# Kernel tuning notes

Measured on AMD Instinct MI355X. Metric: run time of the kernel, lower is better.

Reference implementation:

```python
import jax, jax.numpy as jnp
import numpy as np

NUM_GRAPHS = 256


def _lin_params(key, fan_in, fan_out):
    k1, k2 = jax.random.split(key)
    bound = 1.0 / np.sqrt(fan_in)
    W = jax.random.uniform(k1, (fan_in, fan_out), jnp.float32, -bound, bound)
    b = jax.random.uniform(k2, (fan_out,), jnp.float32, -bound, bound)
    return W, b


def setup_inputs() -> dict:
    key = jax.random.key(0)
    ks = jax.random.split(key, 12)
    N, E, F = 100000, 3200000, 32
    x = jax.random.normal(ks[0], (N, F), jnp.float32)
    edge_index = jax.random.randint(ks[1], (2, E), 0, N, jnp.int64)
    batch = jnp.sort(jax.random.randint(ks[2], (N,), 0, NUM_GRAPHS, jnp.int64))
    W1, b1 = _lin_params(ks[3], 32, 32)   # conv1
    W2, b2 = _lin_params(ks[4], 32, 24)   # conv2
    Wg, bg = _lin_params(ks[5], 24, 32)   # g_fcn1
    Wt, bt = _lin_params(ks[6], 32, 2)    # t_fcn1
    Wn1, bn1 = _lin_params(ks[7], 24, 16)  # n_fcn1
    Wn2, bn2 = _lin_params(ks[8], 16, 1)   # n_fcn2
    Wb1, bb1 = _lin_params(ks[9], 24, 16)  # b_fcn1
    Wb2, bb2 = _lin_params(ks[10], 16, 3)  # b_fcn2
    return {"x": x, "edge_index": edge_index, "batch": batch,
            "W1": W1, "b1": b1, "W2": W2, "b2": b2,
            "Wg": Wg, "bg": bg, "Wt": Wt, "bt": bt,
            "Wn1": Wn1, "bn1": bn1, "Wn2": Wn2, "bn2": bn2,
            "Wb1": Wb1, "bb1": bb1, "Wb2": Wb2, "bb2": bb2}


def _gcn_conv(x, edge_index, W, b):
    """PyG GCNConv: self-loops + symmetric normalization + linear."""
    N = x.shape[0]
    h = x @ W  # [N, out]
    loop = jnp.arange(N, dtype=edge_index.dtype)
    row = jnp.concatenate([edge_index[0], loop])  # source
    col = jnp.concatenate([edge_index[1], loop])  # target
    deg = jax.ops.segment_sum(jnp.ones_like(col, dtype=h.dtype), col, num_segments=N)
    dinv = jnp.where(deg > 0, jax.lax.rsqrt(deg), 0.0)
    norm = dinv[row] * dinv[col]  # [E+N]
    out = jax.ops.segment_sum(h[row] * norm[:, None], col, num_segments=N)
    return out + b


def _segment_softmax(v, seg, num_seg):
    """Softmax over nodes within each graph (leading axis)."""
    m = jax.ops.segment_max(v, seg, num_segments=num_seg)
    e = jnp.exp(v - m[seg])
    s = jax.ops.segment_sum(e, seg, num_segments=num_seg)
    return e / s[seg]


def reference(x, edge_index, batch, W1, b1, W2, b2, Wg, bg, Wt, bt,
              Wn1, bn1, Wn2, bn2, Wb1, bb1, Wb2, bb2):
    h = jax.nn.relu(_gcn_conv(x, edge_index, W1, b1))          # [N,32]
    h = jax.nn.relu(_gcn_conv(h, edge_index, W2, b2))          # [N,24]
    # global mean pool
    cnt = jax.ops.segment_sum(jnp.ones((h.shape[0],), h.dtype), batch, num_segments=NUM_GRAPHS)
    g = jax.ops.segment_sum(h, batch, num_segments=NUM_GRAPHS) / jnp.maximum(cnt, 1.0)[:, None]
    g = g @ Wg + bg                                            # [G,32]
    t = jax.nn.softmax(g @ Wt + bt, axis=1)                    # [G,2]
    n = jax.nn.relu(h @ Wn1 + bn1) @ Wn2 + bn2                 # [N,1]
    n = _segment_softmax(n, batch, NUM_GRAPHS)                 # per-graph softmax over nodes
    b_feat = jax.ops.segment_sum(n * h, batch, num_segments=NUM_GRAPHS)  # global_add_pool of n*x
    bb = jax.nn.relu(b_feat @ Wb1 + bb1) @ Wb2 + bb2           # [G,3]
    bb = jax.nn.softmax(bb, axis=0)                            # dim=0 softmax as in source
    return (t, n, bb)
```

## Files before the change

kernel.cpp:

```cpp
#include <hip/hip_runtime.h>
#include <math.h>

#define NG 256
#define NBLK 256

#define S1F 16.0f
#define IS1F 0.0625f
#define S2F 64.0f
#define IS2F 0.015625f

typedef __attribute__((ext_vector_type(2))) float f32x2;

__device__ __forceinline__ unsigned enc4(float f0, float f1, float f2, float f3) {
    int r = __builtin_amdgcn_cvt_pk_fp8_f32(f0, f1, 0, false);
    r = __builtin_amdgcn_cvt_pk_fp8_f32(f2, f3, r, true);
    return (unsigned)r;
}
__device__ __forceinline__ void acc8p(uint2 v, f32x2 (&a)[4]) {
    a[0] += __builtin_amdgcn_cvt_pk_f32_fp8((int)v.x, false);
    a[1] += __builtin_amdgcn_cvt_pk_f32_fp8((int)v.x, true);
    a[2] += __builtin_amdgcn_cvt_pk_f32_fp8((int)v.y, false);
    a[3] += __builtin_amdgcn_cvt_pk_f32_fp8((int)v.y, true);
}

__global__ __launch_bounds__(256) void hist_bucket_kernel(
        const int* __restrict__ col, int* __restrict__ blockOff,
        int* __restrict__ bucketTot, int E, int NB) {
    __shared__ int h[512];
    h[threadIdx.x] = 0; h[threadIdx.x + 256] = 0;
    __syncthreads();
    const int chunk = (((E + NBLK - 1) / NBLK) + 3) & ~3;
    const int beg = blockIdx.x * chunk;
    const int end = min(beg + chunk, E);
    if ((E & 3) == 0) {
        int e = beg + threadIdx.x * 4;
        for (; e + 3 < end; e += 1024) {
            int4 c = *(const int4*)(col + e);
            atomicAdd(&h[c.x >> 8], 1);
            atomicAdd(&h[c.y >> 8], 1);
            atomicAdd(&h[c.z >> 8], 1);
            atomicAdd(&h[c.w >> 8], 1);
        }
        for (; e < end; e++) atomicAdd(&h[col[e] >> 8], 1);
    } else {
        for (int e = beg + threadIdx.x; e < end; e += 256)
            atomicAdd(&h[col[e] >> 8], 1);
    }
    __syncthreads();
    for (int t = threadIdx.x; t < NB; t += 256) {
        int off = atomicAdd(&bucketTot[t], h[t]);
        blockOff[t * NBLK + blockIdx.x] = off;
    }
}

__global__ __launch_bounds__(512) void tiny_scan_kernel(
        const int* __restrict__ bucketTot, int* __restrict__ bucketBase, int NB) {
    __shared__ int part[512];
    const int t = threadIdx.x;
    int v = (t < NB) ? bucketTot[t] : 0;
    part[t] = v;
    __syncthreads();
    for (int o = 1; o < 512; o <<= 1) {
        int u = (t >= o) ? part[t - o] : 0;
        __syncthreads();
        part[t] += u;
        __syncthreads();
    }
    if (t < NB) bucketBase[t] = part[t] - v;
    if (t == NB) bucketBase[NB] = part[NB - 1];
    if (t == 511 && NB == 512) bucketBase[NB] = part[511];
}

__global__ __launch_bounds__(256) void scatter_pairs_kernel(
        const int* __restrict__ ei, const int* __restrict__ blockOff,
        const int* __restrict__ bucketBase, int* __restrict__ pairs, int E, int NB) {
    __shared__ int cur[512];
    for (int t = threadIdx.x; t < NB; t += 256)
        cur[t] = bucketBase[t] + blockOff[t * NBLK + blockIdx.x];
    __syncthreads();
    const int chunk = (((E + NBLK - 1) / NBLK) + 3) & ~3;
    const int beg = blockIdx.x * chunk;
    const int end = min(beg + chunk, E);
    if ((E & 3) == 0) {
        int e = beg + threadIdx.x * 4;
        for (; e + 3 < end; e += 1024) {
            int4 s = *(const int4*)(ei + e);
            int4 tg = *(const int4*)(ei + E + e);
            int p0 = atomicAdd(&cur[tg.x >> 8], 1);
            pairs[p0] = (int)(((unsigned)(tg.x & 255) << 17) | (unsigned)s.x);
            int p1 = atomicAdd(&cur[tg.y >> 8], 1);
            pairs[p1] = (int)(((unsigned)(tg.y & 255) << 17) | (unsigned)s.y);
            int p2 = atomicAdd(&cur[tg.z >> 8], 1);
            pairs[p2] = (int)(((unsigned)(tg.z & 255) << 17) | (unsigned)s.z);
            int p3 = atomicAdd(&cur[tg.w >> 8], 1);
            pairs[p3] = (int)(((unsigned)(tg.w & 255) << 17) | (unsigned)s.w);
        }
        for (; e < end; e++) {
            int src = ei[e];
            int tgt = ei[E + e];
            int pos = atomicAdd(&cur[tgt >> 8], 1);
            pairs[pos] = (int)(((unsigned)(tgt & 255) << 17) | (unsigned)src);
        }
    } else {
        for (int e = beg + threadIdx.x; e < end; e += 256) {
            int src = ei[e];
            int tgt = ei[E + e];
            int pos = atomicAdd(&cur[tgt >> 8], 1);
            pairs[pos] = (int)(((unsigned)(tgt & 255) << 17) | (unsigned)src);
        }
    }
}

__global__ __launch_bounds__(256) void csr_bucket_kernel(
        const int* __restrict__ pairs, const int* __restrict__ bucketBase,
        int* __restrict__ rowptr, int* __restrict__ adj,
        float* __restrict__ dinv, int N, int E) {
    __shared__ int h[256];
    __shared__ int sc[256];
    __shared__ int cur[256];
    const int b = blockIdx.x, t = threadIdx.x;
    const int base = bucketBase[b];
    const int end = bucketBase[b + 1];
    h[t] = 0;
    __syncthreads();
    for (int i = base + t; i < end; i += 256)
        atomicAdd(&h[(unsigned)pairs[i] >> 17], 1);
    __syncthreads();
    const int v = h[t];
    sc[t] = v;
    __syncthreads();
    for (int o = 1; o < 256; o <<= 1) {
        int u = (t >= o) ? sc[t - o] : 0;
        __syncthreads();
        sc[t] += u;
        __syncthreads();
    }
    const int ex = sc[t] - v;
    const int node = (b << 8) + t;
    if (node < N) {
        rowptr[node] = base + ex;
        dinv[node] = rsqrtf((float)v + 1.0f);
    }
    cur[t] = base + ex;
    __syncthreads();
    for (int i = base + t; i < end; i += 256) {
        unsigned p = (unsigned)pairs[i];
        int pos = atomicAdd(&cur[p >> 17], 1);
        adj[pos] = (int)(p & 0x1FFFFu);
    }
    if (b == 0 && t == 0) rowptr[N] = E;
}

__global__ __launch_bounds__(256) void bounds_kernel(
        const int* __restrict__ batch, int* __restrict__ starts, int N) {
    int i = blockIdx.x * blockDim.x + threadIdx.x;
    if (i >= N) return;
    int b = batch[i];
    int bp = (i == 0) ? -1 : batch[i - 1];
    for (int g = bp + 1; g <= b; g++) starts[g] = i;
    if (i == N - 1)
        for (int g = b + 1; g <= NG; g++) starts[g] = N;
}

__global__ __launch_bounds__(256) void hs1_kernel(
        const float* __restrict__ x, const float* __restrict__ W,
        const float* __restrict__ dinv, unsigned* __restrict__ hs, int N) {
    __shared__ float Ws[32 * 32];
    __shared__ float tmp[8][32];
    for (int t = threadIdx.x; t < 1024; t += blockDim.x) Ws[t] = W[t];
    __syncthreads();
    const int tid = threadIdx.x;
    const int node = blockIdx.x * 8 + (tid >> 5);
    const int n = tid >> 5, f = tid & 31;
    if (node < N) {
        const float* xr = x + (size_t)node * 32;
        float acc = 0.f;
#pragma unroll
        for (int k = 0; k < 32; k++) acc += xr[k] * Ws[k * 32 + f];
        tmp[n][f] = acc * dinv[node] * S1F;
        if (f < 8)
            hs[(size_t)node * 8 + f] = enc4(tmp[n][4 * f], tmp[n][4 * f + 1],
                                            tmp[n][4 * f + 2], tmp[n][4 * f + 3]);
    }
}

__global__ __launch_bounds__(256) void gather1_kernel(
        const int* __restrict__ rowptr, const int* __restrict__ adj,
        const uint2* __restrict__ hs1q, const float* __restrict__ dinv,
        const float* __restrict__ b1, const float* __restrict__ W2,
        unsigned* __restrict__ hs2out, int N) {
    __shared__ float W2s[32 * 24];
    __shared__ float b1s[32];
    __shared__ float h1row[8][32];
    __shared__ float hs2t[8][32];
    const int tid = threadIdx.x;
    for (int t = tid; t < 768; t += 256) W2s[t] = W2[t];
    if (tid < 32) b1s[tid] = b1[tid];

    const int node = blockIdx.x * 8 + (tid >> 5);
    const int n = tid >> 5;
    const int l = tid & 31;
    const int f8 = l & 3;
    const int e8 = l >> 2;
    const bool valid = node < N;

    int beg = 0, cnt = 0;
    if (valid) { beg = rowptr[node]; cnt = rowptr[node + 1] - beg; }
    const int* ap = adj + beg;
    f32x2 a[4];
#pragma unroll
    for (int k = 0; k < 4; k++) { a[k][0] = 0.f; a[k][1] = 0.f; }
    int j = 0;
    for (; j + 32 <= cnt; j += 32) {
        int s0 = ap[j + e8];
        int s1 = ap[j + 8 + e8];
        int s2 = ap[j + 16 + e8];
        int s3 = ap[j + 24 + e8];
        uint2 v0 = hs1q[(size_t)s0 * 4 + f8];
        uint2 v1 = hs1q[(size_t)s1 * 4 + f8];
        uint2 v2 = hs1q[(size_t)s2 * 4 + f8];
        uint2 v3 = hs1q[(size_t)s3 * 4 + f8];
        acc8p(v0, a); acc8p(v1, a); acc8p(v2, a); acc8p(v3, a);
    }
    for (; j + 16 <= cnt; j += 16) {
        int s0 = ap[j + e8];
        int s1 = ap[j + 8 + e8];
        uint2 v0 = hs1q[(size_t)s0 * 4 + f8];
        uint2 v1 = hs1q[(size_t)s1 * 4 + f8];
        acc8p(v0, a); acc8p(v1, a);
    }
    for (; j + 8 <= cnt; j += 8) {
        int s0 = ap[j + e8];
        acc8p(hs1q[(size_t)s0 * 4 + f8], a);
    }
    if (e8 < cnt - j) {
        int s0 = ap[j + e8];
        acc8p(hs1q[(size_t)s0 * 4 + f8], a);
    }
#pragma unroll
    for (int k = 0; k < 4; k++) {
        float x0 = a[k][0], x1 = a[k][1];
        x0 += __shfl_xor(x0, 4); x0 += __shfl_xor(x0, 8); x0 += __shfl_xor(x0, 16);
        x1 += __shfl_xor(x1, 4); x1 += __shfl_xor(x1, 8); x1 += __shfl_xor(x1, 16);
        a[k][0] = x0; a[k][1] = x1;
    }

    __syncthreads();

    float di = 0.f;
    if (valid) {
        di = dinv[node];
        if (e8 == 0) {
            f32x2 s[4];
#pragma unroll
            for (int k = 0; k < 4; k++) { s[k][0] = 0.f; s[k][1] = 0.f; }
            acc8p(hs1q[(size_t)node * 4 + f8], s);
            const float c = di * IS1F;
#pragma unroll
            for (int k = 0; k < 4; k++) {
                h1row[n][8 * f8 + 2 * k]     = fmaxf(c * (a[k][0] + s[k][0]) + b1s[8 * f8 + 2 * k], 0.f);
                h1row[n][8 * f8 + 2 * k + 1] = fmaxf(c * (a[k][1] + s[k][1]) + b1s[8 * f8 + 2 * k + 1], 0.f);
            }
        }
    }
    if (valid) {
        float aa = 0.f;
        if (l < 24) {
#pragma unroll
            for (int k = 0; k < 32; k++) aa += h1row[n][k] * W2s[k * 24 + l];
        }
        hs2t[n][l] = (l < 24) ? aa * di * S2F : 0.f;
        if (l < 8)
            hs2out[(size_t)node * 8 + l] = enc4(hs2t[n][4 * l], hs2t[n][4 * l + 1],
                                                hs2t[n][4 * l + 2], hs2t[n][4 * l + 3]);
    }
}

__global__ __launch_bounds__(256) void gather2_kernel(
        const int* __restrict__ rowptr, const int* __restrict__ adj,
        const uint2* __restrict__ hs2q, const float* __restrict__ dinv,
        const float* __restrict__ b2,
        const float* __restrict__ Wn1, const float* __restrict__ bn1,
        const float* __restrict__ Wn2, const float* __restrict__ bn2,
        float* __restrict__ h2out, float* __restrict__ vout, int N) {
    __shared__ float Wn1s[24 * 16];
    __shared__ float b2s[32], bn1s[16], Wn2s[16];
    __shared__ float h2row[8][32];
    const int tid = threadIdx.x;
    for (int t = tid; t < 384; t += 256) Wn1s[t] = Wn1[t];
    if (tid < 32) b2s[tid] = (tid < 24) ? b2[tid] : 0.f;
    if (tid < 16) { bn1s[tid] = bn1[tid]; Wn2s[tid] = Wn2[tid]; }

    const int node = blockIdx.x * 8 + (tid >> 5);
    const int n = tid >> 5;
    const int l = tid & 31;
    const int f8 = l & 3;
    const int e8 = l >> 2;
    const bool valid = node < N;

    int beg = 0, cnt = 0;
    if (valid) { beg = rowptr[node]; cnt = rowptr[node + 1] - beg; }
    const int* ap = adj + beg;
    f32x2 a[4];
#pragma unroll
    for (int k = 0; k < 4; k++) { a[k][0] = 0.f; a[k][1] = 0.f; }
    int j = 0;
    for (; j + 32 <= cnt; j += 32) {
        int s0 = ap[j + e8];
        int s1 = ap[j + 8 + e8];
        int s2 = ap[j + 16 + e8];
        int s3 = ap[j + 24 + e8];
        uint2 v0 = hs2q[(size_t)s0 * 4 + f8];
        uint2 v1 = hs2q[(size_t)s1 * 4 + f8];
        uint2 v2 = hs2q[(size_t)s2 * 4 + f8];
        uint2 v3 = hs2q[(size_t)s3 * 4 + f8];
        acc8p(v0, a); acc8p(v1, a); acc8p(v2, a); acc8p(v3, a);
    }
    for (; j + 16 <= cnt; j += 16) {
        int s0 = ap[j + e8];
        int s1 = ap[j + 8 + e8];
        uint2 v0 = hs2q[(size_t)s0 * 4 + f8];
        uint2 v1 = hs2q[(size_t)s1 * 4 + f8];
        acc8p(v0, a); acc8p(v1, a);
    }
    for (; j + 8 <= cnt; j += 8) {
        int s0 = ap[j + e8];
        acc8p(hs2q[(size_t)s0 * 4 + f8], a);
    }
    if (e8 < cnt - j) {
        int s0 = ap[j + e8];
        acc8p(hs2q[(size_t)s0 * 4 + f8], a);
    }
#pragma unroll
    for (int k = 0; k < 4; k++) {
        float x0 = a[k][0], x1 = a[k][1];
        x0 += __shfl_xor(x0, 4); x0 += __shfl_xor(x0, 8); x0 += __shfl_xor(x0, 16);
        x1 += __shfl_xor(x1, 4); x1 += __shfl_xor(x1, 8); x1 += __shfl_xor(x1, 16);
        a[k][0] = x0; a[k][1] = x1;
    }

    __syncthreads();

    if (valid && e8 == 0) {
        float di = dinv[node];
        f32x2 s[4];
#pragma unroll
        for (int k = 0; k < 4; k++) { s[k][0] = 0.f; s[k][1] = 0.f; }
        acc8p(hs2q[(size_t)node * 4 + f8], s);
        const float c = di * IS2F;
#pragma unroll
        for (int k = 0; k < 4; k++) {
            h2row[n][8 * f8 + 2 * k]     = fmaxf(c * (a[k][0] + s[k][0]) + b2s[8 * f8 + 2 * k], 0.f);
            h2row[n][8 * f8 + 2 * k + 1] = fmaxf(c * (a[k][1] + s[k][1]) + b2s[8 * f8 + 2 * k + 1], 0.f);
        }
    }
    if (valid && l < 24) h2out[(size_t)node * 24 + l] = h2row[n][l];

    float val = 0.f;
    if (valid && l < 16) {
        float u = bn1s[l];
#pragma unroll
        for (int k = 0; k < 24; k++) u += h2row[n][k] * Wn1s[k * 16 + l];
        val = fmaxf(u, 0.f) * Wn2s[l];
    }
    val += __shfl_down(val, 8, 16);
    val += __shfl_down(val, 4, 16);
    val += __shfl_down(val, 2, 16);
    val += __shfl_down(val, 1, 16);
    if (valid && l == 0) vout[node] = val + bn2[0];
}

__global__ __launch_bounds__(256) void graph_kernel(
        const float* __restrict__ v, const float* __restrict__ h2,
        const int* __restrict__ starts,
        const float* __restrict__ Wg, const float* __restrict__ bg,
        const float* __restrict__ Wt, const float* __restrict__ bt,
        const float* __restrict__ Wb1p, const float* __restrict__ bb1p,
        const float* __restrict__ Wb2p, const float* __restrict__ bb2p,
        float* __restrict__ out_t, float* __restrict__ out_n,
        float* __restrict__ bbpre, int N) {
    const int g = blockIdx.x;
    const int tid = threadIdx.x;
    const int lane = tid & 63;
    const int wv = tid >> 6;

    const int start = starts[g];
    const int end = starts[g + 1];

    __shared__ float sm[4];
    __shared__ float pH[4][24], pW[4][24], pS[4];

    float m = -INFINITY;
    for (int idx = start + tid; idx < end; idx += 256) m = fmaxf(m, v[idx]);
#pragma unroll
    for (int off = 32; off > 0; off >>= 1) m = fmaxf(m, __shfl_down(m, off, 64));
    if (lane == 0) sm[wv] = m;
    __syncthreads();
    m = fmaxf(fmaxf(sm[0], sm[1]), fmaxf(sm[2], sm[3]));

    const int half = lane >> 5;
    const int slot = wv * 2 + half;
    const int feat = lane & 31;
    const bool fa = feat < 24;
    float hs = 0.f, ws = 0.f, se = 0.f;
    int i = start + slot;
    for (; i + 24 < end; i += 32) {
        float v0 = v[i], v1 = v[i + 8], v2 = v[i + 16], v3 = v[i + 24];
        float h0 = 0.f, h1 = 0.f, hh2 = 0.f, h3 = 0.f;
        if (fa) {
            h0 = h2[(size_t)i * 24 + feat];
            h1 = h2[(size_t)(i + 8) * 24 + feat];
            hh2 = h2[(size_t)(i + 16) * 24 + feat];
            h3 = h2[(size_t)(i + 24) * 24 + feat];
        }
        float e0 = __expf(v0 - m), e1 = __expf(v1 - m);
        float e2 = __expf(v2 - m), e3 = __expf(v3 - m);
        if (feat == 0) se += (e0 + e1) + (e2 + e3);
        hs += (h0 + h1) + (hh2 + h3);
        ws += (e0 * h0 + e1 * h1) + (e2 * hh2 + e3 * h3);
    }
    for (; i < end; i += 8) {
        float vv = v[i];
        float e = __expf(vv - m);
        if (feat == 0) se += e;
        if (fa) {
            float hv = h2[(size_t)i * 24 + feat];
            hs += hv;
            ws += e * hv;
        }
    }
    hs += __shfl_xor(hs, 32, 64);
    ws += __shfl_xor(ws, 32, 64);
    se += __shfl_xor(se, 32, 64);
    if (lane < 24) { pH[wv][lane] = hs; pW[wv][lane] = ws; }
    if (lane == 0) pS[wv] = se;
    __syncthreads();
    const float stot = pS[0] + pS[1] + pS[2] + pS[3];
    const float invs = (stot > 0.f) ? 1.f / stot : 0.f;

    for (int idx = start + tid; idx < end; idx += 256)
        out_n[idx] = __expf(v[idx] - m) * invs;

    const float denom = fmaxf((float)(end - start), 1.0f);
    if (tid < 32) {
        float a = bg[tid];
#pragma unroll
        for (int k = 0; k < 24; k++) {
            float mean_k = (pH[0][k] + pH[1][k] + pH[2][k] + pH[3][k]) / denom;
            a += mean_k * Wg[k * 32 + tid];
        }
        float p0 = a * Wt[tid * 2];
        float p1 = a * Wt[tid * 2 + 1];
#pragma unroll
        for (int off = 16; off > 0; off >>= 1) {
            p0 += __shfl_down(p0, off, 32);
            p1 += __shfl_down(p1, off, 32);
        }
        if (tid == 0) {
            float t0 = p0 + bt[0], t1 = p1 + bt[1];
            float tm = fmaxf(t0, t1);
            float e0 = __expf(t0 - tm), e1 = __expf(t1 - tm);
            float ts = e0 + e1;
            out_t[g * 2 + 0] = e0 / ts;
            out_t[g * 2 + 1] = e1 / ts;
        }
    }
    if (tid < 16) {
        float u = bb1p[tid];
#pragma unroll
        for (int k = 0; k < 24; k++) {
            float bf_k = (pW[0][k] + pW[1][k] + pW[2][k] + pW[3][k]) * invs;
            u += bf_k * Wb1p[k * 16 + tid];
        }
        u = fmaxf(u, 0.f);
        float q0 = u * Wb2p[tid * 3 + 0];
        float q1 = u * Wb2p[tid * 3 + 1];
        float q2 = u * Wb2p[tid * 3 + 2];
#pragma unroll
        for (int off = 8; off > 0; off >>= 1) {
            q0 += __shfl_down(q0, off, 16);
            q1 += __shfl_down(q1, off, 16);
            q2 += __shfl_down(q2, off, 16);
        }
        if (tid == 0) {
            bbpre[g * 3 + 0] = q0 + bb2p[0];
            bbpre[g * 3 + 1] = q1 + bb2p[1];
            bbpre[g * 3 + 2] = q2 + bb2p[2];
        }
    }
}

__global__ __launch_bounds__(256) void bb_kernel(
        const float* __restrict__ bbpre, float* __restrict__ out_bb) {
    __shared__ float red[NG];
    int g = threadIdx.x;
#pragma unroll
    for (int c = 0; c < 3; c++) {
        float vv = bbpre[g * 3 + c];
        red[g] = vv;
        __syncthreads();
        for (int off = 128; off > 0; off >>= 1) {
            if (g < off) red[g] = fmaxf(red[g], red[g + off]);
            __syncthreads();
        }
        float m = red[0];
        __syncthreads();
        float e = __expf(vv - m);
        red[g] = e;
        __syncthreads();
        for (int off = 128; off > 0; off >>= 1) {
            if (g < off) red[g] += red[g + off];
            __syncthreads();
        }
        float ssum = red[0];
        __syncthreads();
        out_bb[g * 3 + c] = e / ssum;
    }
}

extern "C" void kernel_launch(void* const* d_in, const int* in_sizes, int n_in,
                              void* d_out, int out_size, void* d_ws, size_t ws_size,
                              hipStream_t stream) {
    const float* x   = (const float*)d_in[0];
    const int*   ei  = (const int*)d_in[1];
    const int*   bat = (const int*)d_in[2];
    const float* W1  = (const float*)d_in[3];
    const float* b1  = (const float*)d_in[4];
    const float* W2  = (const float*)d_in[5];
    const float* b2  = (const float*)d_in[6];
    const float* Wg  = (const float*)d_in[7];
    const float* bg  = (const float*)d_in[8];
    const float* Wt  = (const float*)d_in[9];
    const float* bt  = (const float*)d_in[10];
    const float* Wn1 = (const float*)d_in[11];
    const float* bn1 = (const float*)d_in[12];
    const float* Wn2 = (const float*)d_in[13];
    const float* bn2 = (const float*)d_in[14];
    const float* Wb1 = (const float*)d_in[15];
    const float* bb1 = (const float*)d_in[16];
    const float* Wb2 = (const float*)d_in[17];
    const float* bb2 = (const float*)d_in[18];

    const int N = in_sizes[2];
    const int E = in_sizes[1] / 2;
    const int NB = (N + 255) >> 8;
    const int M = NB * NBLK;

    auto rnd4 = [](size_t v) { return (v + 3) & ~(size_t)3; };
    size_t oRow = 0;
    size_t oDin = oRow + rnd4((size_t)N + 1);
    size_t oAdj = oDin + rnd4((size_t)N);
    size_t oBB  = oAdj + rnd4((size_t)E);
    size_t oTot = oBB + rnd4((size_t)NB + 1);
    size_t oSt  = oTot + rnd4((size_t)NB);
    size_t oT   = oSt + rnd4((size_t)NG + 1);
    size_t oPar = oT + rnd4((size_t)M);

    int*   wsi     = (int*)d_ws;
    float* wsf     = (float*)d_ws;
    int*   rowptr  = wsi + oRow;
    float* dinv    = wsf + oDin;
    int*   adj     = wsi + oAdj;
    int*   bbase   = wsi + oBB;
    int*   btot    = wsi + oTot;
    int*   starts  = wsi + oSt;
    int*   blkoff  = wsi + oT;
    int*   pairs   = wsi + oPar;
    unsigned* hs1b = (unsigned*)(wsf + oT);
    float* h2      = wsf + oT;
    float* vbuf    = wsf + oT + (size_t)24 * N;
    unsigned* hs2b = (unsigned*)(wsf + oT + (size_t)26 * N);
    float* bbpre   = wsf + oT + (size_t)28 * N;

    float* out_t  = (float*)d_out;
    float* out_n  = out_t + 2 * NG;
    float* out_bb = out_t + 2 * NG + N;

    const int B = 256;

    (void)hipMemsetAsync(btot, 0, (size_t)NB * sizeof(int), stream);
    bounds_kernel<<<(N + B - 1) / B, B, 0, stream>>>(bat, starts, N);
    hist_bucket_kernel<<<NBLK, B, 0, stream>>>(ei + E, blkoff, btot, E, NB);
    tiny_scan_kernel<<<1, 512, 0, stream>>>(btot, bbase, NB);
    scatter_pairs_kernel<<<NBLK, B, 0, stream>>>(ei, blkoff, bbase, pairs, E, NB);
    csr_bucket_kernel<<<NB, B, 0, stream>>>(pairs, bbase, rowptr, adj, dinv, N, E);

    hs1_kernel<<<(N + 7) / 8, B, 0, stream>>>(x, W1, dinv, hs1b, N);
    gather1_kernel<<<(N + 7) / 8, B, 0, stream>>>(rowptr, adj, (const uint2*)hs1b,
                                                  dinv, b1, W2, hs2b, N);
    gather2_kernel<<<(N + 7) / 8, B, 0, stream>>>(rowptr, adj, (const uint2*)hs2b,
                                                  dinv, b2, Wn1, bn1, Wn2, bn2, h2, vbuf, N);
    graph_kernel<<<NG, B, 0, stream>>>(vbuf, h2, starts, Wg, bg, Wt, bt,
                                       Wb1, bb1, Wb2, bb2, out_t, out_n, bbpre, N);
    bb_kernel<<<1, B, 0, stream>>>(bbpre, out_bb);
}
```

Measured before the change: 299.0 us.

## Process two nodes per 32-lane group in GCN gather kernels for more loads in flight

Each 32-lane group in both gather kernels now aggregates two destination nodes at once, interleaving their neighbor-index and feature loads in a single padded loop of 32 neighbors per iteration. The former tail loops become masked loads, where lanes past a node's degree read node 0 and have the value zeroed. The aim is more independent memory requests in flight per wave and half as many blocks, to hide gather latency. In exchange, each pass runs to the larger of the two degrees, wasting lanes and issuing redundant loads, and register pressure goes up.

```diff
diff --git a/kernel.cpp b/kernel.cpp
--- a/kernel.cpp
+++ b/kernel.cpp
@@ -191,88 +191,108 @@
         unsigned* __restrict__ hs2out, int N) {
     __shared__ float W2s[32 * 24];
     __shared__ float b1s[32];
-    __shared__ float h1row[8][32];
-    __shared__ float hs2t[8][32];
+    __shared__ float h1row[16][32];
+    __shared__ float hs2t[16][32];
     const int tid = threadIdx.x;
     for (int t = tid; t < 768; t += 256) W2s[t] = W2[t];
     if (tid < 32) b1s[tid] = b1[tid];
 
-    const int node = blockIdx.x * 8 + (tid >> 5);
-    const int n = tid >> 5;
+    const int g = tid >> 5;
     const int l = tid & 31;
     const int f8 = l & 3;
     const int e8 = l >> 2;
-    const bool valid = node < N;
-
-    int beg = 0, cnt = 0;
-    if (valid) { beg = rowptr[node]; cnt = rowptr[node + 1] - beg; }
-    const int* ap = adj + beg;
-    f32x2 a[4];
-#pragma unroll
-    for (int k = 0; k < 4; k++) { a[k][0] = 0.f; a[k][1] = 0.f; }
-    int j = 0;
-    for (; j + 32 <= cnt; j += 32) {
-        int s0 = ap[j + e8];
-        int s1 = ap[j + 8 + e8];
-        int s2 = ap[j + 16 + e8];
-        int s3 = ap[j + 24 + e8];
-        uint2 v0 = hs1q[(size_t)s0 * 4 + f8];
-        uint2 v1 = hs1q[(size_t)s1 * 4 + f8];
-        uint2 v2 = hs1q[(size_t)s2 * 4 + f8];
-        uint2 v3 = hs1q[(size_t)s3 * 4 + f8];
-        acc8p(v0, a); acc8p(v1, a); acc8p(v2, a); acc8p(v3, a);
-    }
-    for (; j + 16 <= cnt; j += 16) {
-        int s0 = ap[j + e8];
-        int s1 = ap[j + 8 + e8];
-        uint2 v0 = hs1q[(size_t)s0 * 4 + f8];
-        uint2 v1 = hs1q[(size_t)s1 * 4 + f8];
-        acc8p(v0, a); acc8p(v1, a);
-    }
-    for (; j + 8 <= cnt; j += 8) {
-        int s0 = ap[j + e8];
-        acc8p(hs1q[(size_t)s0 * 4 + f8], a);
-    }
-    if (e8 < cnt - j) {
-        int s0 = ap[j + e8];
-        acc8p(hs1q[(size_t)s0 * 4 + f8], a);
+    const int n0 = (blockIdx.x * 8 + g) * 2;
+    const int n1 = n0 + 1;
+    const bool val0 = n0 < N;
+    const bool val1 = n1 < N;
+
+    int beg0 = 0, cnt0 = 0, beg1 = 0, cnt1 = 0;
+    if (val0) {
+        int2 rp = *(const int2*)(rowptr + n0);
+        beg0 = rp.x; cnt0 = rp.y - rp.x;
+        if (val1) { int e2 = rowptr[n0 + 2]; beg1 = rp.y; cnt1 = e2 - rp.y; }
+    }
+    const int* ap0 = adj + beg0;
+    const int* ap1 = adj + beg1;
+    f32x2 a0[4], a1[4];
+#pragma unroll
+    for (int k = 0; k < 4; k++) { a0[k][0] = 0.f; a0[k][1] = 0.f; a1[k][0] = 0.f; a1[k][1] = 0.f; }
+
+    const int jmax = max(cnt0, cnt1);
+    for (int j = 0; j < jmax; j += 32) {
+        const int i0 = j + e8, i1 = j + 8 + e8, i2 = j + 16 + e8, i3 = j + 24 + e8;
+        int sA0 = ap0[i0], sA1 = ap0[i1], sA2 = ap0[i2], sA3 = ap0[i3];
+        int sB0 = ap1[i0], sB1 = ap1[i1], sB2 = ap1[i2], sB3 = ap1[i3];
+        if (i0 >= cnt0) sA0 = 0; if (i1 >= cnt0) sA1 = 0;
+        if (i2 >= cnt0) sA2 = 0; if (i3 >= cnt0) sA3 = 0;
+        if (i0 >= cnt1) sB0 = 0; if (i1 >= cnt1) sB1 = 0;
+        if (i2 >= cnt1) sB2 = 0; if (i3 >= cnt1) sB3 = 0;
+        uint2 vA0 = hs1q[(size_t)sA0 * 4 + f8];
+        uint2 vA1 = hs1q[(size_t)sA1 * 4 + f8];
+        uint2 vA2 = hs1q[(size_t)sA2 * 4 + f8];
+        uint2 vA3 = hs1q[(size_t)sA3 * 4 + f8];
+        uint2 vB0 = hs1q[(size_t)sB0 * 4 + f8];
+        uint2 vB1 = hs1q[(size_t)sB1 * 4 + f8];
+        uint2 vB2 = hs1q[(size_t)sB2 * 4 + f8];
+        uint2 vB3 = hs1q[(size_t)sB3 * 4 + f8];
+        if (i0 >= cnt0) { vA0.x = 0u; vA0.y = 0u; }
+        if (i1 >= cnt0) { vA1.x = 0u; vA1.y = 0u; }
+        if (i2 >= cnt0) { vA2.x = 0u; vA2.y = 0u; }
+        if (i3 >= cnt0) { vA3.x = 0u; vA3.y = 0u; }
+        if (i0 >= cnt1) { vB0.x = 0u; vB0.y = 0u; }
+        if (i1 >= cnt1) { vB1.x = 0u; vB1.y = 0u; }
+        if (i2 >= cnt1) { vB2.x = 0u; vB2.y = 0u; }
+        if (i3 >= cnt1) { vB3.x = 0u; vB3.y = 0u; }
+        acc8p(vA0, a0); acc8p(vA1, a0); acc8p(vA2, a0); acc8p(vA3, a0);
+        acc8p(vB0, a1); acc8p(vB1, a1); acc8p(vB2, a1); acc8p(vB3, a1);
     }
 #pragma unroll
     for (int k = 0; k < 4; k++) {
-        float x0 = a[k][0], x1 = a[k][1];
+        float x0 = a0[k][0], x1 = a0[k][1], y0 = a1[k][0], y1 = a1[k][1];
         x0 += __shfl_xor(x0, 4); x0 += __shfl_xor(x0, 8); x0 += __shfl_xor(x0, 16);
         x1 += __shfl_xor(x1, 4); x1 += __shfl_xor(x1, 8); x1 += __shfl_xor(x1, 16);
-        a[k][0] = x0; a[k][1] = x1;
-    }
-
-    __syncthreads();
-
-    float di = 0.f;
-    if (valid) {
-        di = dinv[node];
-        if (e8 == 0) {
-            f32x2 s[4];
-#pragma unroll
-            for (int k = 0; k < 4; k++) { s[k][0] = 0.f; s[k][1] = 0.f; }
-            acc8p(hs1q[(size_t)node * 4 + f8], s);
-            const float c = di * IS1F;
-#pragma unroll
-            for (int k = 0; k < 4; k++) {
-                h1row[n][8 * f8 + 2 * k]     = fmaxf(c * (a[k][0] + s[k][0]) + b1s[8 * f8 + 2 * k], 0.f);
-                h1row[n][8 * f8 + 2 * k + 1] = fmaxf(c * (a[k][1] + s[k][1]) + b1s[8 * f8 + 2 * k + 1], 0.f);
-            }
-        }
-    }
-    if (valid) {
+        y0 += __shfl_xor(y0, 4); y0 += __shfl_xor(y0, 8); y0 += __shfl_xor(y0, 16);
+        y1 += __shfl_xor(y1, 4); y1 += __shfl_xor(y1, 8); y1 += __shfl_xor(y1, 16);
+        a0[k][0] = x0; a0[k][1] = x1; a1[k][0] = y0; a1[k][1] = y1;
+    }
+
+    __syncthreads();
+
+    auto fin1 = [&](const f32x2 (&a)[4], int node, int row) {
+        const int fq = l & 3;
+        const float c = dinv[node] * IS1F;
+        uint2 w = hs1q[(size_t)node * 4 + fq];
+        f32x2 s0 = __builtin_amdgcn_cvt_pk_f32_fp8((int)w.x, false);
+        f32x2 s1 = __builtin_amdgcn_cvt_pk_f32_fp8((int)w.x, true);
+        f32x2 s2 = __builtin_amdgcn_cvt_pk_f32_fp8((int)w.y, false);
+        f32x2 s3 = __builtin_amdgcn_cvt_pk_f32_fp8((int)w.y, true);
+        h1row[row][8 * fq + 0] = fmaxf(c * (a[0][0] + s0[0]) + b1s[8 * fq + 0], 0.f);
+        h1row[row][8 * fq + 1] = fmaxf(c * (a[0][1] + s0[1]) + b1s[8 * fq + 1], 0.f);
+        h1row[row][8 * fq + 2] = fmaxf(c * (a[1][0] + s1[0]) + b1s[8 * fq + 2], 0.f);
+        h1row[row][8 * fq + 3] = fmaxf(c * (a[1][1] + s1[1]) + b1s[8 * fq + 3], 0.f);
+        h1row[row][8 * fq + 4] = fmaxf(c * (a[2][0] + s2[0]) + b1s[8 * fq + 4], 0.f);
+        h1row[row][8 * fq + 5] = fmaxf(c * (a[2][1] + s2[1]) + b1s[8 * fq + 5], 0.f);
+        h1row[row][8 * fq + 6] = fmaxf(c * (a[3][0] + s3[0]) + b1s[8 * fq + 6], 0.f);
+        h1row[row][8 * fq + 7] = fmaxf(c * (a[3][1] + s3[1]) + b1s[8 * fq + 7], 0.f);
+    };
+    if (l < 4) { if (val0) fin1(a0, n0, 2 * g); }
+    else if (l < 8) { if (val1) fin1(a1, n1, 2 * g + 1); }
+
+#pragma unroll
+    for (int nn = 0; nn < 2; ++nn) {
+        const int node = n0 + nn;
+        if (node >= N) break;
+        const int row = 2 * g + nn;
+        const float sc = dinv[node] * S2F;
         float aa = 0.f;
         if (l < 24) {
 #pragma unroll
-            for (int k = 0; k < 32; k++) aa += h1row[n][k] * W2s[k * 24 + l];
-        }
-        hs2t[n][l] = (l < 24) ? aa * di * S2F : 0.f;
+            for (int k = 0; k < 32; k++) aa += h1row[row][k] * W2s[k * 24 + l];
+        }
+        hs2t[row][l] = (l < 24) ? aa * sc : 0.f;
         if (l < 8)
-            hs2out[(size_t)node * 8 + l] = enc4(hs2t[n][4 * l], hs2t[n][4 * l + 1],
-                                                hs2t[n][4 * l + 2], hs2t[n][4 * l + 3]);
+            hs2out[(size_t)node * 8 + l] = enc4(hs2t[row][4 * l], hs2t[row][4 * l + 1],
+                                                hs2t[row][4 * l + 2], hs2t[row][4 * l + 3]);
     }
 }
 
@@ -285,89 +305,112 @@
         float* __restrict__ h2out, float* __restrict__ vout, int N) {
     __shared__ float Wn1s[24 * 16];
     __shared__ float b2s[32], bn1s[16], Wn2s[16];
-    __shared__ float h2row[8][32];
+    __shared__ float h2row[16][32];
     const int tid = threadIdx.x;
     for (int t = tid; t < 384; t += 256) Wn1s[t] = Wn1[t];
     if (tid < 32) b2s[tid] = (tid < 24) ? b2[tid] : 0.f;
     if (tid < 16) { bn1s[tid] = bn1[tid]; Wn2s[tid] = Wn2[tid]; }
 
-    const int node = blockIdx.x * 8 + (tid >> 5);
-    const int n = tid >> 5;
+    const int g = tid >> 5;
     const int l = tid & 31;
     const int f8 = l & 3;
     const int e8 = l >> 2;
-    const bool valid = node < N;
-
-    int beg = 0, cnt = 0;
-    if (valid) { beg = rowptr[node]; cnt = rowptr[node + 1] - beg; }
-    const int* ap = adj + beg;
-    f32x2 a[4];
-#pragma unroll
-    for (int k = 0; k < 4; k++) { a[k][0] = 0.f; a[k][1] = 0.f; }
-    int j = 0;
-    for (; j + 32 <= cnt; j += 32) {
-        int s0 = ap[j + e8];
-        int s1 = ap[j + 8 + e8];
-        int s2 = ap[j + 16 + e8];
-        int s3 = ap[j + 24 + e8];
-        uint2 v0 = hs2q[(size_t)s0 * 4 + f8];
-        uint2 v1 = hs2q[(size_t)s1 * 4 + f8];
-        uint2 v2 = hs2q[(size_t)s2 * 4 + f8];
-        uint2 v3 = hs2q[(size_t)s3 * 4 + f8];
-        acc8p(v0, a); acc8p(v1, a); acc8p(v2, a); acc8p(v3, a);
-    }
-    for (; j + 16 <= cnt; j += 16) {
-        int s0 = ap[j + e8];
-        int s1 = ap[j + 8 + e8];
-        uint2 v0 = hs2q[(size_t)s0 * 4 + f8];
-        uint2 v1 = hs2q[(size_t)s1 * 4 + f8];
-        acc8p(v0, a); acc8p(v1, a);
-    }
-    for (; j + 8 <= cnt; j += 8) {
-        int s0 = ap[j + e8];
-        acc8p(hs2q[(size_t)s0 * 4 + f8], a);
-    }
-    if (e8 < cnt - j) {
-        int s0 = ap[j + e8];
-        acc8p(hs2q[(size_t)s0 * 4 + f8], a);
+    const int n0 = (blockIdx.x * 8 + g) * 2;
+    const int n1 = n0 + 1;
+    const bool val0 = n0 < N;
+    const bool val1 = n1 < N;
+
+    int beg0 = 0, cnt0 = 0, beg1 = 0, cnt1 = 0;
+    if (val0) {
+        int2 rp = *(const int2*)(rowptr + n0);
+        beg0 = rp.x; cnt0 = rp.y - rp.x;
+        if (val1) { int e2 = rowptr[n0 + 2]; beg1 = rp.y; cnt1 = e2 - rp.y; }
+    }
+    const int* ap0 = adj + beg0;
+    const int* ap1 = adj + beg1;
+    f32x2 a0[4], a1[4];
+#pragma unroll
+    for (int k = 0; k < 4; k++) { a0[k][0] = 0.f; a0[k][1] = 0.f; a1[k][0] = 0.f; a1[k][1] = 0.f; }
+
+    const int jmax = max(cnt0, cnt1);
+    for (int j = 0; j < jmax; j += 32) {
+        const int i0 = j + e8, i1 = j + 8 + e8, i2 = j + 16 + e8, i3 = j + 24 + e8;
+        int sA0 = ap0[i0], sA1 = ap0[i1], sA2 = ap0[i2], sA3 = ap0[i3];
+        int sB0 = ap1[i0], sB1 = ap1[i1], sB2 = ap1[i2], sB3 = ap1[i3];
+        if (i0 >= cnt0) sA0 = 0; if (i1 >= cnt0) sA1 = 0;
+        if (i2 >= cnt0) sA2 = 0; if (i3 >= cnt0) sA3 = 0;
+        if (i0 >= cnt1) sB0 = 0; if (i1 >= cnt1) sB1 = 0;
+        if (i2 >= cnt1) sB2 = 0; if (i3 >= cnt1) sB3 = 0;
+        uint2 vA0 = hs2q[(size_t)sA0 * 4 + f8];
+        uint2 vA1 = hs2q[(size_t)sA1 * 4 + f8];
+        uint2 vA2 = hs2q[(size_t)sA2 * 4 + f8];
+        uint2 vA3 = hs2q[(size_t)sA3 * 4 + f8];
+        uint2 vB0 = hs2q[(size_t)sB0 * 4 + f8];
+        uint2 vB1 = hs2q[(size_t)sB1 * 4 + f8];
+        uint2 vB2 = hs2q[(size_t)sB2 * 4 + f8];
+        uint2 vB3 = hs2q[(size_t)sB3 * 4 + f8];
+        if (i0 >= cnt0) { vA0.x = 0u; vA0.y = 0u; }
+        if (i1 >= cnt0) { vA1.x = 0u; vA1.y = 0u; }
+        if (i2 >= cnt0) { vA2.x = 0u; vA2.y = 0u; }
+        if (i3 >= cnt0) { vA3.x = 0u; vA3.y = 0u; }
+        if (i0 >= cnt1) { vB0.x = 0u; vB0.y = 0u; }
+        if (i1 >= cnt1) { vB1.x = 0u; vB1.y = 0u; }
+        if (i2 >= cnt1) { vB2.x = 0u; vB2.y = 0u; }
+        if (i3 >= cnt1) { vB3.x = 0u; vB3.y = 0u; }
+        acc8p(vA0, a0); acc8p(vA1, a0); acc8p(vA2, a0); acc8p(vA3, a0);
+        acc8p(vB0, a1); acc8p(vB1, a1); acc8p(vB2, a1); acc8p(vB3, a1);
     }
 #pragma unroll
     for (int k = 0; k < 4; k++) {
-        float x0 = a[k][0], x1 = a[k][1];
+        float x0 = a0[k][0], x1 = a0[k][1], y0 = a1[k][0], y1 = a1[k][1];
         x0 += __shfl_xor(x0, 4); x0 += __shfl_xor(x0, 8); x0 += __shfl_xor(x0, 16);
         x1 += __shfl_xor(x1, 4); x1 += __shfl_xor(x1, 8); x1 += __shfl_xor(x1, 16);
-        a[k][0] = x0; a[k][1] = x1;
-    }
-
-    __syncthreads();
-
-    if (valid && e8 == 0) {
-        float di = dinv[node];
-        f32x2 s[4];
-#pragma unroll
-        for (int k = 0; k < 4; k++) { s[k][0] = 0.f; s[k][1] = 0.f; }
-        acc8p(hs2q[(size_t)node * 4 + f8], s);
-        const float c = di * IS2F;
-#pragma unroll
-        for (int k = 0; k < 4; k++) {
-            h2row[n][8 * f8 + 2 * k]     = fmaxf(c * (a[k][0] + s[k][0]) + b2s[8 * f8 + 2 * k], 0.f);
-            h2row[n][8 * f8 + 2 * k + 1] = fmaxf(c * (a[k][1] + s[k][1]) + b2s[8 * f8 + 2 * k + 1], 0.f);
-        }
-    }
-    if (valid && l < 24) h2out[(size_t)node * 24 + l] = h2row[n][l];
-
-    float val = 0.f;
-    if (valid && l < 16) {
-        float u = bn1s[l];
-#pragma unroll
-        for (int k = 0; k < 24; k++) u += h2row[n][k] * Wn1s[k * 16 + l];
-        val = fmaxf(u, 0.f) * Wn2s[l];
-    }
-    val += __shfl_down(val, 8, 16);
-    val += __shfl_down(val, 4, 16);
-    val += __shfl_down(val, 2, 16);
-    val += __shfl_down(val, 1, 16);
-    if (valid && l == 0) vout[node] = val + bn2[0];
+        y0 += __shfl_xor(y0, 4); y0 += __shfl_xor(y0, 8); y0 += __shfl_xor(y0, 16);
+        y1 += __shfl_xor(y1, 4); y1 += __shfl_xor(y1, 8); y1 += __shfl_xor(y1, 16);
+        a0[k][0] = x0; a0[k][1] = x1; a1[k][0] = y0; a1[k][1] = y1;
+    }
+
+    __syncthreads();
+
+    auto fin2 = [&](const f32x2 (&a)[4], int node, int row) {
+        const int fq = l & 3;
+        const float c = dinv[node] * IS2F;
+        uint2 w = hs2q[(size_t)node * 4 + fq];
+        f32x2 s0 = __builtin_amdgcn_cvt_pk_f32_fp8((int)w.x, false);
+        f32x2 s1 = __builtin_amdgcn_cvt_pk_f32_fp8((int)w.x, true);
+        f32x2 s2 = __builtin_amdgcn_cvt_pk_f32_fp8((int)w.y, false);
+        f32x2 s3 = __builtin_amdgcn_cvt_pk_f32_fp8((int)w.y, true);
+        h2row[row][8 * fq + 0] = fmaxf(c * (a[0][0] + s0[0]) + b2s[8 * fq + 0], 0.f);
+        h2row[row][8 * fq + 1] = fmaxf(c * (a[0][1] + s0[1]) + b2s[8 * fq + 1], 0.f);
+        h2row[row][8 * fq + 2] = fmaxf(c * (a[1][0] + s1[0]) + b2s[8 * fq + 2], 0.f);
+        h2row[row][8 * fq + 3] = fmaxf(c * (a[1][1] + s1[1]) + b2s[8 * fq + 3], 0.f);
+        h2row[row][8 * fq + 4] = fmaxf(c * (a[2][0] + s2[0]) + b2s[8 * fq + 4], 0.f);
+        h2row[row][8 * fq + 5] = fmaxf(c * (a[2][1] + s2[1]) + b2s[8 * fq + 5], 0.f);
+        h2row[row][8 * fq + 6] = fmaxf(c * (a[3][0] + s3[0]) + b2s[8 * fq + 6], 0.f);
+        h2row[row][8 * fq + 7] = fmaxf(c * (a[3][1] + s3[1]) + b2s[8 * fq + 7], 0.f);
+    };
+    if (l < 4) { if (val0) fin2(a0, n0, 2 * g); }
+    else if (l < 8) { if (val1) fin2(a1, n1, 2 * g + 1); }
+
+#pragma unroll
+    for (int nn = 0; nn < 2; ++nn) {
+        const int node = n0 + nn;
+        if (node >= N) break;
+        const int row = 2 * g + nn;
+        if (l < 24) h2out[(size_t)node * 24 + l] = h2row[row][l];
+        float val = 0.f;
+        if (l < 16) {
+            float u = bn1s[l];
+#pragma unroll
+            for (int k = 0; k < 24; k++) u += h2row[row][k] * Wn1s[k * 16 + l];
+            val = fmaxf(u, 0.f) * Wn2s[l];
+        }
+        val += __shfl_down(val, 8, 16);
+        val += __shfl_down(val, 4, 16);
+        val += __shfl_down(val, 2, 16);
+        val += __shfl_down(val, 1, 16);
+        if (l == 0) vout[node] = val + bn2[0];
+    }
 }
 
 __global__ __launch_bounds__(256) void graph_kernel(
@@ -586,10 +629,10 @@
     csr_bucket_kernel<<<NB, B, 0, stream>>>(pairs, bbase, rowptr, adj, dinv, N, E);
 
     hs1_kernel<<<(N + 7) / 8, B, 0, stream>>>(x, W1, dinv, hs1b, N);
-    gather1_kernel<<<(N + 7) / 8, B, 0, stream>>>(rowptr, adj, (const uint2*)hs1b,
-                                                  dinv, b1, W2, hs2b, N);
-    gather2_kernel<<<(N + 7) / 8, B, 0, stream>>>(rowptr, adj, (const uint2*)hs2b,
-                                                  dinv, b2, Wn1, bn1, Wn2, bn2, h2, vbuf, N);
+    gather1_kernel<<<(N + 15) / 16, B, 0, stream>>>(rowptr, adj, (const uint2*)hs1b,
+                                                    dinv, b1, W2, hs2b, N);
+    gather2_kernel<<<(N + 15) / 16, B, 0, stream>>>(rowptr, adj, (const uint2*)hs2b,
+                                                    dinv, b2, Wn1, bn1, Wn2, bn2, h2, vbuf, N);
     graph_kernel<<<NG, B, 0, stream>>>(vbuf, h2, starts, Wg, bg, Wt, bt,
                                        Wb1, bb1, Wb2, bb2, out_t, out_n, bbpre, N);
     bb_kernel<<<1, B, 0, stream>>>(bbpre, out_bb);
```

Result: faster. 281.0 us (-6.0%).
